# Optimization experiments

Measured on AMD Instinct MI355X. Metric: run time of the kernel, lower is better.

The kernel has to match this reference:

```python
import jax, jax.numpy as jnp
import numpy as np

N = 100000   # nodes
E = 1600000  # edges
D = 128      # feature dim (layers all 128)
G = 512      # graphs in batch
C = 10       # num_classes
EPS = 1e-5   # batchnorm eps


def setup_inputs() -> dict:
    key = jax.random.key(0)
    ks = jax.random.split(key, 16)
    s = 1.0 / np.sqrt(D)
    return {
        "x": jax.random.normal(ks[0], (N, D), jnp.float32),
        "edge_index": jax.random.randint(ks[1], (2, E), 0, N),
        "batch": jnp.sort(jax.random.randint(ks[2], (N,), 0, G)),
        "w1": jax.random.normal(ks[3], (D, D), jnp.float32) * s,
        "b1": jnp.zeros((D,), jnp.float32),
        "w2": jax.random.normal(ks[4], (D, D), jnp.float32) * s,
        "b2": jnp.zeros((D,), jnp.float32),
        "w3": jax.random.normal(ks[5], (D, D), jnp.float32) * s,
        "b3": jnp.zeros((D,), jnp.float32),
        "g1": jnp.ones((D,), jnp.float32),
        "be1": jnp.zeros((D,), jnp.float32),
        "g2": jnp.ones((D,), jnp.float32),
        "be2": jnp.zeros((D,), jnp.float32),
        "fc_w": jax.random.normal(ks[6], (D, C), jnp.float32) * s,
        "fc_b": jnp.zeros((C,), jnp.float32),
    }


def _gcn(x, src, dst, norm, W, b):
    # transform -> gather -> normalize -> scatter-add (PyG GCNConv)
    h = x @ W
    out = jax.ops.segment_sum(h[src] * norm[:, None], dst, num_segments=x.shape[0])
    return out + b


def _bn(x, g, b):
    # training-mode BatchNorm1d: batch mean / biased variance
    mu = jnp.mean(x, axis=0)
    var = jnp.mean((x - mu) ** 2, axis=0)
    return (x - mu) * jax.lax.rsqrt(var + EPS) * g + b


def reference(x, edge_index, batch, w1, b1, w2, b2, w3, b3, g1, be1, g2, be2, fc_w, fc_b):
    n = x.shape[0]
    loop = jnp.arange(n)
    src = jnp.concatenate([edge_index[0], loop])  # add self-loops
    dst = jnp.concatenate([edge_index[1], loop])
    deg = jax.ops.segment_sum(jnp.ones_like(src, x.dtype), dst, num_segments=n)
    dinv = jax.lax.rsqrt(jnp.maximum(deg, 1.0))  # deg >= 1 due to self-loops
    norm = dinv[src] * dinv[dst]  # symmetric normalization per edge

    h = jax.nn.relu(_gcn(x, src, dst, norm, w1, b1))        # conv1 + relu (bn1 unused, per source)
    h = jax.nn.relu(_gcn(h, src, dst, norm, w2, b2))        # conv2 + relu
    h = jax.nn.relu(_bn(h, g1, be1))                        # bn + relu
    h = jax.nn.relu(_gcn(h, src, dst, norm, w3, b3))        # conv3 + relu
    h = jax.nn.relu(_bn(h, g2, be2))                        # bn + relu

    cnt = jax.ops.segment_sum(jnp.ones((n,), h.dtype), batch, num_segments=G)
    pooled = jax.ops.segment_sum(h, batch, num_segments=G) / jnp.maximum(cnt, 1.0)[:, None]
    logits = pooled @ fc_w + fc_b
    return jax.nn.log_softmax(logits, axis=1)
```

## Files before the change

kernel.cpp:

```cpp
#include <hip/hip_runtime.h>
#include <hip/hip_bf16.h>
#include <math.h>

#define D 128
#define G_GRAPHS 512
#define C_CLASSES 10
#define BN_EPS 1e-5f
#define NBUCK_MAX 512
#define EDGE_CHUNK 4096
#define EPT 16

typedef unsigned short u16;
typedef unsigned int u32;
typedef unsigned short ushort4_t __attribute__((ext_vector_type(4)));
typedef unsigned short ushort8_t __attribute__((ext_vector_type(8)));
typedef __bf16 bf16x8 __attribute__((ext_vector_type(8)));
typedef float floatx4 __attribute__((ext_vector_type(4)));
union B8 { ushort8_t u; bf16x8 b; };

__device__ __forceinline__ float bf_lo(u32 v) { return __uint_as_float(v << 16); }
__device__ __forceinline__ float bf_hi(u32 v) { return __uint_as_float(v & 0xffff0000u); }
__device__ __forceinline__ u16 f2bf(float f) {
    union { float f; u32 u; } x; x.f = f;
    u32 r = x.u + 0x7fff + ((x.u >> 16) & 1);
    return (u16)(r >> 16);
}
__device__ __forceinline__ u32 pack2bf(float a, float b) {
    return (u32)f2bf(a) | ((u32)f2bf(b) << 16);
}


__global__ __launch_bounds__(256) void bucket_hist_kernel(
    const int* __restrict__ dst, int* __restrict__ bucketCnt, int E, int nbuck)
{
    __shared__ int h[NBUCK_MAX];
    int tid = threadIdx.x;
    for (int i = tid; i < NBUCK_MAX; i += 256) h[i] = 0;
    __syncthreads();
    for (int i = blockIdx.x * 256 + tid; i < E; i += gridDim.x * 256)
        atomicAdd(&h[dst[i] >> 8], 1);
    __syncthreads();
    for (int i = tid; i < nbuck; i += 256)
        if (h[i]) atomicAdd(&bucketCnt[i], h[i]);
}

__global__ void scan_buckets_kernel(
    const int* __restrict__ bucketCnt, int* __restrict__ bucketBase,
    int* __restrict__ bucketCursor, int* __restrict__ rowPtr, int nbuck, int N, int E)
{
    __shared__ int buf[2][512];
    int tid = threadIdx.x;
    int v = (tid < nbuck) ? bucketCnt[tid] : 0;
    buf[0][tid] = v;
    __syncthreads();
    int cur = 0;
    for (int off = 1; off < 512; off <<= 1) {
        buf[1 - cur][tid] = buf[cur][tid] + ((tid >= off) ? buf[cur][tid - off] : 0);
        cur ^= 1;
        __syncthreads();
    }
    if (tid < nbuck) {
        int b = buf[cur][tid] - v;
        bucketBase[tid] = b;
        bucketCursor[tid] = b;
    }
    if (tid == 0) { bucketBase[nbuck] = E; rowPtr[N] = E; }
}

__global__ __launch_bounds__(256) void scatter_pairs_kernel(
    const int* __restrict__ src, const int* __restrict__ dst,
    int* __restrict__ bucketCursor, u32* __restrict__ pairs, int E)
{
    __shared__ int h[NBUCK_MAX];
    __shared__ int base[NBUCK_MAX];
    int tid = threadIdx.x;
    int e0 = blockIdx.x * EDGE_CHUNK;
    for (int i = tid; i < NBUCK_MAX; i += 256) h[i] = 0;
    __syncthreads();
    int s[EPT], d[EPT], r[EPT];
#pragma unroll
    for (int j = 0; j < EPT; ++j) {
        int i = e0 + j * 256 + tid;
        if (i < E) {
            s[j] = src[i];
            d[j] = dst[i];
            r[j] = atomicAdd(&h[d[j] >> 8], 1);
        } else {
            d[j] = -1;
        }
    }
    __syncthreads();
    for (int i = tid; i < NBUCK_MAX; i += 256)
        if (h[i]) base[i] = atomicAdd(&bucketCursor[i], h[i]);
    __syncthreads();
#pragma unroll
    for (int j = 0; j < EPT; ++j) {
        if (d[j] >= 0) {
            int b = d[j] >> 8;
            pairs[base[b] + r[j]] = ((u32)s[j] << 8) | (u32)(d[j] & 255);
        }
    }
}

__global__ __launch_bounds__(256) void bucket_sort_kernel(
    const u32* __restrict__ pairs, const int* __restrict__ bucketBase,
    int* __restrict__ colIdx, int* __restrict__ rowPtr, float* __restrict__ dinv, int N)
{
    __shared__ int h[256];
    __shared__ int cur[256];
    __shared__ int sbuf[2][256];
    int tid = threadIdx.x;
    int b = blockIdx.x;
    int s = bucketBase[b], e = bucketBase[b + 1];
    h[tid] = 0;
    __syncthreads();
    for (int i = s + tid; i < e; i += 256)
        atomicAdd(&h[pairs[i] & 255], 1);
    __syncthreads();
    int cnt = h[tid];
    sbuf[0][tid] = cnt;
    __syncthreads();
    int c = 0;
    for (int off = 1; off < 256; off <<= 1) {
        sbuf[1 - c][tid] = sbuf[c][tid] + ((tid >= off) ? sbuf[c][tid - off] : 0);
        c ^= 1;
        __syncthreads();
    }
    int excl = sbuf[c][tid] - cnt;
    int v = b * 256 + tid;
    if (v < N) {
        rowPtr[v] = s + excl;
        dinv[v] = rsqrtf((float)(cnt + 1));
    }
    cur[tid] = s + excl;
    __syncthreads();
    for (int i = s + tid; i < e; i += 256) {
        u32 p = pairs[i];
        int pos = atomicAdd(&cur[p & 255], 1);
        colIdx[pos] = (int)(p >> 8);
    }
}

__global__ __launch_bounds__(256) void graph_bounds_kernel(
    const int* __restrict__ batch, int* __restrict__ gstart, int N)
{
    int i = blockIdx.x * 256 + threadIdx.x;
    if (i >= N) return;
    int b = batch[i];
    int prev = (i == 0) ? -1 : batch[i - 1];
    if (b != prev) {
        for (int g = prev + 1; g <= b; ++g) gstart[g] = i;
    }
    if (i == N - 1) {
        for (int g = b + 1; g <= G_GRAPHS; ++g) gstart[g] = N;
    }
}

__global__ __launch_bounds__(256) void wconv_kernel(
    const float4* __restrict__ w1, const float4* __restrict__ w2,
    const float4* __restrict__ w3, u16* __restrict__ wtAll)
{
    const float4* W = (blockIdx.x == 0) ? w1 : (blockIdx.x == 1) ? w2 : w3;
    u16* Wt = wtAll + (size_t)blockIdx.x * D * D;
    int tid = threadIdx.x;
#pragma unroll
    for (int i = 0; i < 16; ++i) {
        int idx = tid + i * 256;
        int k = idx >> 5, c4 = idx & 31;
        float4 v = W[idx];
        Wt[(4 * c4 + 0) * D + k] = f2bf(v.x);
        Wt[(4 * c4 + 1) * D + k] = f2bf(v.y);
        Wt[(4 * c4 + 2) * D + k] = f2bf(v.z);
        Wt[(4 * c4 + 3) * D + k] = f2bf(v.w);
    }
}

#define XS_STRIDE 136
#define GEMM_GRID 768

__device__ __forceinline__ void gemm_core_and_store(
    const u16* Xs, const u16* Ws, u16* __restrict__ Y, int row0, int nrows, int tid)
{
    int wid = tid >> 6, lane = tid & 63;
    int m = lane & 15, quad = lane >> 4;
    int xrow = wid * 16 + m;

    floatx4 acc[8] = {};
#pragma unroll
    for (int ks = 0; ks < 4; ++ks) {
        int kk = ks * 32 + quad * 8;
        B8 a;
        a.u = *(const ushort8_t*)&Xs[xrow * XS_STRIDE + kk];
#pragma unroll
        for (int t = 0; t < 8; ++t) {
            B8 b;
            b.u = *(const ushort8_t*)&Ws[(t * 16 + m) * XS_STRIDE + kk];
            acc[t] = __builtin_amdgcn_mfma_f32_16x16x32_bf16(b.b, a.b, acc[t], 0, 0, 0);
        }
    }
    int grow = row0 + xrow;
    if (grow < nrows) {
#pragma unroll
        for (int t = 0; t < 8; ++t) {
            ushort4_t o;
            o.x = f2bf(acc[t][0]); o.y = f2bf(acc[t][1]);
            o.z = f2bf(acc[t][2]); o.w = f2bf(acc[t][3]);
            *(ushort4_t*)&Y[(size_t)grow * D + t * 16 + quad * 4] = o;
        }
    }
}

__device__ __forceinline__ void stage_w(const u16* __restrict__ Wt, u16* Ws, int tid) {
    const ushort8_t* Wv = (const ushort8_t*)Wt;
#pragma unroll
    for (int i = 0; i < 8; ++i) {
        int idx = tid + i * 256;
        int n = idx >> 4, c8 = idx & 15;
        *(ushort8_t*)&Ws[n * XS_STRIDE + c8 * 8] = Wv[idx];
    }
}

__global__ __launch_bounds__(256) void gemm_mfma_f32in_kernel(
    const float4* __restrict__ X, const u16* __restrict__ Wt,
    u16* __restrict__ Y, int nrows, int ntiles)
{
    __shared__ __align__(16) u16 Xs[64 * XS_STRIDE];
    __shared__ __align__(16) u16 Ws[128 * XS_STRIDE];
    int tid = threadIdx.x;
    stage_w(Wt, Ws, tid);
    for (int t = blockIdx.x; t < ntiles; t += gridDim.x) {
        int row0 = t * 64;
        __syncthreads();
#pragma unroll
        for (int i = 0; i < 8; ++i) {
            int idx = tid + i * 256;
            int r = idx >> 5, c4 = idx & 31;
            int gr = row0 + r;
            float4 v = make_float4(0.f, 0.f, 0.f, 0.f);
            if (gr < nrows) v = X[(size_t)gr * 32 + c4];
            ushort4_t o;
            o.x = f2bf(v.x); o.y = f2bf(v.y); o.z = f2bf(v.z); o.w = f2bf(v.w);
            *(ushort4_t*)&Xs[r * XS_STRIDE + c4 * 4] = o;
        }
        __syncthreads();
        gemm_core_and_store(Xs, Ws, Y, row0, nrows, tid);
    }
}

__global__ __launch_bounds__(256) void gemm_mfma_bf16in_kernel(
    const uint4* __restrict__ X, const u16* __restrict__ Wt,
    const float* __restrict__ gsum, const float* __restrict__ gsq,
    const float* __restrict__ gamma, const float* __restrict__ beta, float invN,
    u16* __restrict__ Y, int nrows, int ntiles)
{
    __shared__ __align__(16) u16 Xs[64 * XS_STRIDE];
    __shared__ __align__(16) u16 Ws[128 * XS_STRIDE];
    __shared__ float scs[D], shs[D];
    int tid = threadIdx.x;
    bool fuse = (gsum != nullptr);
    stage_w(Wt, Ws, tid);
    if (fuse && tid < D) {
        float mu = gsum[tid] * invN;
        float var = gsq[tid] * invN - mu * mu;
        float sc = gamma[tid] * rsqrtf(var + BN_EPS);
        scs[tid] = sc;
        shs[tid] = beta[tid] - mu * sc;
    }
    for (int t = blockIdx.x; t < ntiles; t += gridDim.x) {
        int row0 = t * 64;
        __syncthreads();
#pragma unroll
        for (int i = 0; i < 4; ++i) {
            int idx = tid + i * 256;
            int r = idx >> 4, c8 = idx & 15;
            int gr = row0 + r;
            uint4 v = make_uint4(0, 0, 0, 0);
            if (gr < nrows) v = X[(size_t)gr * 16 + c8];
            if (fuse) {
                int k = c8 * 8;
                v.x = pack2bf(fmaxf(bf_lo(v.x) * scs[k]     + shs[k],     0.f),
                              fmaxf(bf_hi(v.x) * scs[k + 1] + shs[k + 1], 0.f));
                v.y = pack2bf(fmaxf(bf_lo(v.y) * scs[k + 2] + shs[k + 2], 0.f),
                              fmaxf(bf_hi(v.y) * scs[k + 3] + shs[k + 3], 0.f));
                v.z = pack2bf(fmaxf(bf_lo(v.z) * scs[k + 4] + shs[k + 4], 0.f),
                              fmaxf(bf_hi(v.z) * scs[k + 5] + shs[k + 5], 0.f));
                v.w = pack2bf(fmaxf(bf_lo(v.w) * scs[k + 6] + shs[k + 6], 0.f),
                              fmaxf(bf_hi(v.w) * scs[k + 7] + shs[k + 7], 0.f));
            }
            *(uint4*)&Xs[r * XS_STRIDE + c8 * 8] = v;
        }
        __syncthreads();
        gemm_core_and_store(Xs, Ws, Y, row0, nrows, tid);
    }
}

#define ACC8(tw, duu)                                              \
    acc[0] += (duu) * bf_lo((tw).x); acc[1] += (duu) * bf_hi((tw).x); \
    acc[2] += (duu) * bf_lo((tw).y); acc[3] += (duu) * bf_hi((tw).y); \
    acc[4] += (duu) * bf_lo((tw).z); acc[5] += (duu) * bf_hi((tw).z); \
    acc[6] += (duu) * bf_lo((tw).w); acc[7] += (duu) * bf_hi((tw).w);

__global__ __launch_bounds__(256) void aggregate_kernel(
    const uint4* __restrict__ T, const int* __restrict__ colIdx,
    const int* __restrict__ rowPtr, const float* __restrict__ dinv,
    const float* __restrict__ bias, u32* __restrict__ outH, int n)
{
    int wid = threadIdx.x >> 6;
    int lane = threadIdx.x & 63;
    int row = blockIdx.x * 4 + wid;
    if (row >= n) return;
    int fg = lane & 15;
    int eg = lane >> 4;
    const char* baseT = (const char*)T + fg * 16;

    float dr = dinv[row];
    float acc[8] = {};

    if (eg == 0) {
        uint4 sv = T[(size_t)row * 16 + fg];
        acc[0] = dr * bf_lo(sv.x); acc[1] = dr * bf_hi(sv.x);
        acc[2] = dr * bf_lo(sv.y); acc[3] = dr * bf_hi(sv.y);
        acc[4] = dr * bf_lo(sv.z); acc[5] = dr * bf_hi(sv.z);
        acc[6] = dr * bf_lo(sv.w); acc[7] = dr * bf_hi(sv.w);
    }

    int s = rowPtr[row], e = rowPtr[row + 1];
    for (int j0 = s; j0 < e; j0 += 64) {
        int m = e - j0;
        if (m > 64) m = 64;
        u32 voff = (u32)row << 8;
        float du = 0.f;
        if (lane < m) {
            int u = colIdx[j0 + lane];
            voff = (u32)u << 8;
            du = dinv[u];
        }
        int nc = (m + 15) >> 4;
        for (int c = 0; c < nc; ++c) {
            int b0 = c * 16 + eg;
            u32 o0 = (u32)__shfl((int)voff, b0);      u32 o1 = (u32)__shfl((int)voff, b0 + 4);
            u32 o2 = (u32)__shfl((int)voff, b0 + 8);  u32 o3 = (u32)__shfl((int)voff, b0 + 12);
            float d0 = __shfl(du, b0);      float d1 = __shfl(du, b0 + 4);
            float d2 = __shfl(du, b0 + 8);  float d3 = __shfl(du, b0 + 12);
            uint4 t0 = *(const uint4*)(baseT + o0);
            uint4 t1 = *(const uint4*)(baseT + o1);
            uint4 t2 = *(const uint4*)(baseT + o2);
            uint4 t3 = *(const uint4*)(baseT + o3);
            ACC8(t0, d0); ACC8(t1, d1); ACC8(t2, d2); ACC8(t3, d3);
        }
    }

#pragma unroll
    for (int off = 16; off < 64; off <<= 1) {
#pragma unroll
        for (int i = 0; i < 8; ++i) acc[i] += __shfl_xor(acc[i], off);
    }

    const float2* bp = (const float2*)bias;
    int pidx = fg * 4 + eg;
    float2 b = bp[pidx];
    float ox = fmaxf(dr * acc[eg * 2] + b.x, 0.f);
    float oy = fmaxf(dr * acc[eg * 2 + 1] + b.y, 0.f);
    outH[(size_t)row * 64 + pidx] = pack2bf(ox, oy);
}

__global__ __launch_bounds__(256) void bn_stats_kernel(
    const u32* __restrict__ H, int n, float* __restrict__ gsum, float* __restrict__ gsq)
{
    int tid = threadIdx.x;
    int c = tid & 63, rr = tid >> 6;
    float sA = 0.f, sA2 = 0.f, sB = 0.f, sB2 = 0.f;
    for (int row = blockIdx.x * 4 + rr; row < n; row += gridDim.x * 4) {
        u32 v = H[(size_t)row * 64 + c];
        float a = bf_lo(v), b = bf_hi(v);
        sA += a; sA2 += a * a; sB += b; sB2 += b * b;
    }
    __shared__ float shA[256], shA2[256], shB[256], shB2[256];
    shA[tid] = sA; shA2[tid] = sA2; shB[tid] = sB; shB2[tid] = sB2;
    __syncthreads();
    if (tid < 64) {
        float tA = shA[tid] + shA[tid + 64] + shA[tid + 128] + shA[tid + 192];
        float tA2 = shA2[tid] + shA2[tid + 64] + shA2[tid + 128] + shA2[tid + 192];
        float tB = shB[tid] + shB[tid + 64] + shB[tid + 128] + shB[tid + 192];
        float tB2 = shB2[tid] + shB2[tid + 64] + shB2[tid + 128] + shB2[tid + 192];
        atomicAdd(&gsum[2 * c], tA);
        atomicAdd(&gsq[2 * c], tA2);
        atomicAdd(&gsum[2 * c + 1], tB);
        atomicAdd(&gsq[2 * c + 1], tB2);
    }
}

__global__ __launch_bounds__(256) void pool_classify_kernel(
    const u32* __restrict__ H, const float* __restrict__ gsum, const float* __restrict__ gsq,
    const float* __restrict__ gamma, const float* __restrict__ beta, float invN,
    const int* __restrict__ gstart, const float* __restrict__ fcw,
    const float* __restrict__ fcb, float* __restrict__ out)
{
    int g = blockIdx.x;
    int tid = threadIdx.x;
    int c = tid & 63, q = tid >> 6;
    float muA = gsum[2 * c] * invN, muB = gsum[2 * c + 1] * invN;
    float vA = gsq[2 * c] * invN - muA * muA, vB = gsq[2 * c + 1] * invN - muB * muB;
    float scA = gamma[2 * c] * rsqrtf(vA + BN_EPS), scB = gamma[2 * c + 1] * rsqrtf(vB + BN_EPS);
    float shA = beta[2 * c] - muA * scA, shB = beta[2 * c + 1] - muB * scB;

    int s = gstart[g], cnt = gstart[g + 1] - s;
    float aA = 0.f, aB = 0.f;
    for (int i = q; i < cnt; i += 4) {
        u32 v = H[(size_t)(s + i) * 64 + c];
        aA += fmaxf(bf_lo(v) * scA + shA, 0.f);
        aB += fmaxf(bf_hi(v) * scB + shB, 0.f);
    }
    __shared__ float sA[256], sB[256];
    __shared__ float prow[D];
    __shared__ float lg[C_CLASSES];
    sA[tid] = aA; sB[tid] = aB;
    __syncthreads();
    if (tid < 64) {
        float tA = sA[tid] + sA[tid + 64] + sA[tid + 128] + sA[tid + 192];
        float tB = sB[tid] + sB[tid + 64] + sB[tid + 128] + sB[tid + 192];
        float inv = 1.f / (float)(cnt > 1 ? cnt : 1);
        prow[2 * tid] = tA * inv;
        prow[2 * tid + 1] = tB * inv;
    }
    __syncthreads();
    if (tid < C_CLASSES) {
        float sum = fcb[tid];
        for (int d = 0; d < D; ++d) sum += prow[d] * fcw[d * C_CLASSES + tid];
        lg[tid] = sum;
    }
    __syncthreads();
    if (tid == 0) {
        float mx = -1e30f;
        for (int k = 0; k < C_CLASSES; ++k) mx = fmaxf(mx, lg[k]);
        float se = 0.f;
        for (int k = 0; k < C_CLASSES; ++k) se += expf(lg[k] - mx);
        float lse = mx + logf(se);
        for (int k = 0; k < C_CLASSES; ++k) out[(size_t)g * C_CLASSES + k] = lg[k] - lse;
    }
}

extern "C" void kernel_launch(void* const* d_in, const int* in_sizes, int n_in,
                              void* d_out, int out_size, void* d_ws, size_t ws_size,
                              hipStream_t stream) {
    const float* x   = (const float*)d_in[0];
    const int* ei    = (const int*)d_in[1];
    const int* batch = (const int*)d_in[2];
    const float* w1  = (const float*)d_in[3];
    const float* b1  = (const float*)d_in[4];
    const float* w2  = (const float*)d_in[5];
    const float* b2  = (const float*)d_in[6];
    const float* w3  = (const float*)d_in[7];
    const float* b3  = (const float*)d_in[8];
    const float* g1  = (const float*)d_in[9];
    const float* be1 = (const float*)d_in[10];
    const float* g2  = (const float*)d_in[11];
    const float* be2 = (const float*)d_in[12];
    const float* fcw = (const float*)d_in[13];
    const float* fcb = (const float*)d_in[14];

    const int N = in_sizes[0] / D;
    const int E = in_sizes[1] / 2;
    const int* src = ei;
    const int* dst = ei + E;
    const int nbuck = (N + 255) >> 8;
    const float invN = 1.f / (float)N;

    char* p = (char*)d_ws;
    auto alloc = [&](size_t bytes) -> void* {
        void* r = (void*)p;
        p += (bytes + 255) & ~(size_t)255;
        return r;
    };
    int*   bucketCnt    = (int*)alloc(NBUCK_MAX * 4);
    float* statsacc     = (float*)alloc(4 * D * 4);
    float* gsum1 = statsacc, *gsq1 = statsacc + D, *gsum2 = statsacc + 2 * D, *gsq2 = statsacc + 3 * D;
    float* dinv     = (float*)alloc((size_t)N * 4);
    int*   rowPtr   = (int*)alloc((size_t)(N + 1) * 4);
    int*   colIdx   = (int*)alloc((size_t)E * 4);
    u32*   pairs    = (u32*)alloc((size_t)E * 4);
    int*   bucketBase   = (int*)alloc((NBUCK_MAX + 1) * 4);
    int*   bucketCursor = (int*)alloc(NBUCK_MAX * 4);
    int*   gstart  = (int*)alloc((G_GRAPHS + 1) * 4);
    u16*   wtAll   = (u16*)alloc((size_t)3 * D * D * 2);
    u16*   tmp     = (u16*)alloc((size_t)N * D * 2);
    u16*   hbuf    = (u16*)alloc((size_t)N * D * 2);

    hipMemsetAsync(bucketCnt, 0, NBUCK_MAX * 4 + 4 * D * 4, stream);

    bucket_hist_kernel<<<512, 256, 0, stream>>>(dst, bucketCnt, E, nbuck);
    scan_buckets_kernel<<<1, 512, 0, stream>>>(bucketCnt, bucketBase, bucketCursor, rowPtr, nbuck, N, E);
    scatter_pairs_kernel<<<(E + EDGE_CHUNK - 1) / EDGE_CHUNK, 256, 0, stream>>>(src, dst, bucketCursor, pairs, E);
    bucket_sort_kernel<<<nbuck, 256, 0, stream>>>(pairs, bucketBase, colIdx, rowPtr, dinv, N);
    graph_bounds_kernel<<<(N + 255) / 256, 256, 0, stream>>>(batch, gstart, N);
    wconv_kernel<<<3, 256, 0, stream>>>((const float4*)w1, (const float4*)w2, (const float4*)w3, wtAll);

    const int NT = (N + 63) / 64;
    const int GB = NT < GEMM_GRID ? NT : GEMM_GRID;
    const int AB = (N + 3) / 4;

    gemm_mfma_f32in_kernel<<<GB, 256, 0, stream>>>((const float4*)x, wtAll, tmp, N, NT);
    aggregate_kernel<<<AB, 256, 0, stream>>>((const uint4*)tmp, colIdx, rowPtr, dinv, b1, (u32*)hbuf, N);
    gemm_mfma_bf16in_kernel<<<GB, 256, 0, stream>>>((const uint4*)hbuf, wtAll + D * D,
        nullptr, nullptr, nullptr, nullptr, 0.f, tmp, N, NT);
    aggregate_kernel<<<AB, 256, 0, stream>>>((const uint4*)tmp, colIdx, rowPtr, dinv, b2, (u32*)hbuf, N);
    bn_stats_kernel<<<256, 256, 0, stream>>>((const u32*)hbuf, N, gsum1, gsq1);
    gemm_mfma_bf16in_kernel<<<GB, 256, 0, stream>>>((const uint4*)hbuf, wtAll + 2 * D * D,
        gsum1, gsq1, g1, be1, invN, tmp, N, NT);
    aggregate_kernel<<<AB, 256, 0, stream>>>((const uint4*)tmp, colIdx, rowPtr, dinv, b3, (u32*)hbuf, N);
    bn_stats_kernel<<<256, 256, 0, stream>>>((const u32*)hbuf, N, gsum2, gsq2);
    pool_classify_kernel<<<G_GRAPHS, 256, 0, stream>>>((const u32*)hbuf, gsum2, gsq2, g2, be2, invN,
        gstart, fcw, fcb, (float*)d_out);
}
```

Measured before the change: 510.2 us.

## Assign one row per 16-lane group in GCN aggregation instead of per wavefront

The aggregation kernel now maps four destination rows to each wavefront, one per 16-lane group, rather than spreading one row's edges across all 64 lanes. This drops the cross-group shuffle reduction and writes each row's output as full 16-byte vectors. With about 17 edges per row, most of the old wavefront's lanes sat idle. The cost is more divergence between groups whose rows have different degrees, and fewer independent gathers in flight per row.

After: 515.2 us. About the same (+1.0%).

```diff
diff --git a/kernel.cpp b/kernel.cpp
--- a/kernel.cpp
+++ b/kernel.cpp
@@ -303,20 +303,22 @@
 __global__ __launch_bounds__(256) void aggregate_kernel(
     const uint4* __restrict__ T, const int* __restrict__ colIdx,
     const int* __restrict__ rowPtr, const float* __restrict__ dinv,
-    const float* __restrict__ bias, u32* __restrict__ outH, int n)
+    const float* __restrict__ bias, uint4* __restrict__ outH, int n)
 {
     int wid = threadIdx.x >> 6;
     int lane = threadIdx.x & 63;
-    int row = blockIdx.x * 4 + wid;
-    if (row >= n) return;
     int fg = lane & 15;
     int eg = lane >> 4;
-    const char* baseT = (const char*)T + fg * 16;
-
-    float dr = dinv[row];
+    int row = (blockIdx.x * 4 + wid) * 4 + eg;
+    bool active = row < n;
+
+    float dr = 0.f;
+    int s = 0, m = 0;
     float acc[8] = {};
-
-    if (eg == 0) {
+    if (active) {
+        dr = dinv[row];
+        s = rowPtr[row];
+        m = rowPtr[row + 1] - s;
         uint4 sv = T[(size_t)row * 16 + fg];
         acc[0] = dr * bf_lo(sv.x); acc[1] = dr * bf_hi(sv.x);
         acc[2] = dr * bf_lo(sv.y); acc[3] = dr * bf_hi(sv.y);
@@ -324,44 +326,40 @@
         acc[6] = dr * bf_lo(sv.w); acc[7] = dr * bf_hi(sv.w);
     }
 
-    int s = rowPtr[row], e = rowPtr[row + 1];
-    for (int j0 = s; j0 < e; j0 += 64) {
-        int m = e - j0;
-        if (m > 64) m = 64;
-        u32 voff = (u32)row << 8;
+    for (int c0 = 0; c0 < m; c0 += 16) {
+        int mm = m - c0;
+        if (mm > 16) mm = 16;
+        int u = row;
         float du = 0.f;
-        if (lane < m) {
-            int u = colIdx[j0 + lane];
-            voff = (u32)u << 8;
+        if (fg < mm) {
+            u = colIdx[s + c0 + fg];
             du = dinv[u];
         }
-        int nc = (m + 15) >> 4;
-        for (int c = 0; c < nc; ++c) {
-            int b0 = c * 16 + eg;
-            u32 o0 = (u32)__shfl((int)voff, b0);      u32 o1 = (u32)__shfl((int)voff, b0 + 4);
-            u32 o2 = (u32)__shfl((int)voff, b0 + 8);  u32 o3 = (u32)__shfl((int)voff, b0 + 12);
-            float d0 = __shfl(du, b0);      float d1 = __shfl(du, b0 + 4);
-            float d2 = __shfl(du, b0 + 8);  float d3 = __shfl(du, b0 + 12);
-            uint4 t0 = *(const uint4*)(baseT + o0);
-            uint4 t1 = *(const uint4*)(baseT + o1);
-            uint4 t2 = *(const uint4*)(baseT + o2);
-            uint4 t3 = *(const uint4*)(baseT + o3);
+        int nb = (mm + 3) >> 2;
+        for (int b = 0; b < nb; ++b) {
+            int base = (eg << 4) + (b << 2);
+            int u0 = __shfl(u, base);     float d0 = __shfl(du, base);
+            int u1 = __shfl(u, base + 1); float d1 = __shfl(du, base + 1);
+            int u2 = __shfl(u, base + 2); float d2 = __shfl(du, base + 2);
+            int u3 = __shfl(u, base + 3); float d3 = __shfl(du, base + 3);
+            uint4 t0 = T[(size_t)u0 * 16 + fg];
+            uint4 t1 = T[(size_t)u1 * 16 + fg];
+            uint4 t2 = T[(size_t)u2 * 16 + fg];
+            uint4 t3 = T[(size_t)u3 * 16 + fg];
             ACC8(t0, d0); ACC8(t1, d1); ACC8(t2, d2); ACC8(t3, d3);
         }
     }
 
-#pragma unroll
-    for (int off = 16; off < 64; off <<= 1) {
-#pragma unroll
-        for (int i = 0; i < 8; ++i) acc[i] += __shfl_xor(acc[i], off);
-    }
-
-    const float2* bp = (const float2*)bias;
-    int pidx = fg * 4 + eg;
-    float2 b = bp[pidx];
-    float ox = fmaxf(dr * acc[eg * 2] + b.x, 0.f);
-    float oy = fmaxf(dr * acc[eg * 2 + 1] + b.y, 0.f);
-    outH[(size_t)row * 64 + pidx] = pack2bf(ox, oy);
+    if (active) {
+        const float4* bp = (const float4*)bias;
+        float4 b0 = bp[fg * 2], b1 = bp[fg * 2 + 1];
+        uint4 o;
+        o.x = pack2bf(fmaxf(dr * acc[0] + b0.x, 0.f), fmaxf(dr * acc[1] + b0.y, 0.f));
+        o.y = pack2bf(fmaxf(dr * acc[2] + b0.z, 0.f), fmaxf(dr * acc[3] + b0.w, 0.f));
+        o.z = pack2bf(fmaxf(dr * acc[4] + b1.x, 0.f), fmaxf(dr * acc[5] + b1.y, 0.f));
+        o.w = pack2bf(fmaxf(dr * acc[6] + b1.z, 0.f), fmaxf(dr * acc[7] + b1.w, 0.f));
+        outH[(size_t)row * 16 + fg] = o;
+    }
 }
 
 __global__ __launch_bounds__(256) void bn_stats_kernel(
@@ -497,17 +495,17 @@
 
     const int NT = (N + 63) / 64;
     const int GB = NT < GEMM_GRID ? NT : GEMM_GRID;
-    const int AB = (N + 3) / 4;
+    const int AB = (N + 15) / 16;
 
     gemm_mfma_f32in_kernel<<<GB, 256, 0, stream>>>((const float4*)x, wtAll, tmp, N, NT);
-    aggregate_kernel<<<AB, 256, 0, stream>>>((const uint4*)tmp, colIdx, rowPtr, dinv, b1, (u32*)hbuf, N);
+    aggregate_kernel<<<AB, 256, 0, stream>>>((const uint4*)tmp, colIdx, rowPtr, dinv, b1, (uint4*)hbuf, N);
     gemm_mfma_bf16in_kernel<<<GB, 256, 0, stream>>>((const uint4*)hbuf, wtAll + D * D,
         nullptr, nullptr, nullptr, nullptr, 0.f, tmp, N, NT);
-    aggregate_kernel<<<AB, 256, 0, stream>>>((const uint4*)tmp, colIdx, rowPtr, dinv, b2, (u32*)hbuf, N);
+    aggregate_kernel<<<AB, 256, 0, stream>>>((const uint4*)tmp, colIdx, rowPtr, dinv, b2, (uint4*)hbuf, N);
     bn_stats_kernel<<<256, 256, 0, stream>>>((const u32*)hbuf, N, gsum1, gsq1);
     gemm_mfma_bf16in_kernel<<<GB, 256, 0, stream>>>((const uint4*)hbuf, wtAll + 2 * D * D,
         gsum1, gsq1, g1, be1, invN, tmp, N, NT);
-    aggregate_kernel<<<AB, 256, 0, stream>>>((const uint4*)tmp, colIdx, rowPtr, dinv, b3, (u32*)hbuf, N);
+    aggregate_kernel<<<AB, 256, 0, stream>>>((const uint4*)tmp, colIdx, rowPtr, dinv, b3, (uint4*)hbuf, N);
     bn_stats_kernel<<<256, 256, 0, stream>>>((const u32*)hbuf, N, gsum2, gsq2);
     pool_classify_kernel<<<G_GRAPHS, 256, 0, stream>>>((const u32*)hbuf, gsum2, gsq2, g2, be2, invN,
         gstart, fcw, fcb, (float*)d_out);
```
